# Kernel optimization log

Measured on AMD Instinct MI355X. Metric: run time of the kernel, lower is better.

Reference implementation:

```python
import jax, jax.numpy as jnp
import numpy as np

EPS = 1e-5      # eps used in abs() and log()
BN_EPS = 1e-5   # torch BatchNorm2d default eps


def setup_inputs() -> dict:
    key = jax.random.key(0)
    ks = jax.random.split(key, 5)
    N, C, F, T = 16, 4, 257, 1000
    B, K = 8, 80
    xr = jax.random.normal(ks[0], (N, C, F, T), dtype=jnp.float32)
    xi = jax.random.normal(ks[1], (N, C, F, T), dtype=jnp.float32)
    # per-bin complex beamforming weights: (F, B, C) == Conv1d weight (B*F, 1, C) regrouped
    wr = jax.random.normal(ks[2], (F, B, C), dtype=jnp.float32) * 0.25
    wi = jax.random.normal(ks[3], (F, B, C), dtype=jnp.float32) * 0.25
    # nn.Linear(num_bins, spectra_filters, bias=False) weight: (K, F)
    w_proj = jax.random.normal(ks[4], (K, F), dtype=jnp.float32) * (1.0 / np.sqrt(F))
    gamma = jnp.ones((B,), dtype=jnp.float32)
    beta = jnp.zeros((B,), dtype=jnp.float32)
    return {"xr": xr, "xi": xi, "wr": wr, "wi": wi, "w_proj": w_proj,
            "gamma": gamma, "beta": beta}


def reference(xr, xi, wr, wi, w_proj, gamma, beta):
    # Grouped complex conv1d == per-bin complex beamform across mics:
    # out[n,b,t,f] = sum_c w[f,b,c] * x[n,c,f,t] (complex product)
    br = jnp.einsum('ncft,fbc->nbtf', xr, wr) - jnp.einsum('ncft,fbc->nbtf', xi, wi)
    bi = jnp.einsum('ncft,fbc->nbtf', xi, wr) + jnp.einsum('ncft,fbc->nbtf', xr, wi)
    mag = jnp.sqrt(br * br + bi * bi + EPS)              # (N, B, T, F)
    # Linear(F -> K), ReLU, log
    f = jax.nn.relu(jnp.einsum('nbtf,kf->nbtk', mag, w_proj))
    f = jnp.log(f + EPS)                                  # (N, B, T, K)
    # BatchNorm2d over channel axis B (training-mode batch statistics)
    mean = jnp.mean(f, axis=(0, 2, 3), keepdims=True)
    var = jnp.var(f, axis=(0, 2, 3), keepdims=True)
    f = (f - mean) * jax.lax.rsqrt(var + BN_EPS)
    f = f * gamma[None, :, None, None] + beta[None, :, None, None]
    N, B, T, K = f.shape
    # (N, B, T, K) -> (N, T, B*K)
    return jnp.transpose(f, (0, 2, 1, 3)).reshape(N, T, B * K)
```

## Files before the change

### kernel.cpp

```cpp
#include <hip/hip_runtime.h>
#include <math.h>

#define N_ 16
#define C_ 4
#define F_ 257
#define T_ 1000
#define B_ 8
#define K_ 80
#define BK_ 640
#define TT_ 16
#define NT_ 63
#define NBLK (N_ * NT_)
#define MSTR 264

typedef _Float16 half4 __attribute__((ext_vector_type(4)));
typedef _Float16 half8 __attribute__((ext_vector_type(8)));
typedef float f32x4 __attribute__((ext_vector_type(4)));

#define WSCALE   256.0f
#define WUNSCALE 0.00390625f

#define WP0_OFF   0
#define WP1_OFF   (64 * 1024)
#define WP2_OFF   (128 * 1024)
#define WTAIL_OFF (192 * 1024)
#define PART_OFF  (256 * 1024)
#define SS_OFF    (PART_OFF + NBLK * 16 * 8)

__global__ __launch_bounds__(80) void k_wt(const float* __restrict__ wp,
                                           _Float16* __restrict__ wp0,
                                           _Float16* __restrict__ wp1,
                                           _Float16* __restrict__ wp2,
                                           float* __restrict__ wtail) {
    int blk = blockIdx.x;
    int tid = threadIdx.x;
    if (blk < 80) {
        if (tid < 64) {
            int ch = blk / 10, r = blk % 10, kt = r >> 1, ksub = r & 1;
            int k = kt * 16 + (tid & 15);
            int fb = ch * 32 + ksub * 16 + 4 * (tid >> 4);
#pragma unroll
            for (int j = 0; j < 4; ++j) {
                float w = wp[k * F_ + fb + j] * WSCALE;
                _Float16 w0 = (_Float16)w;
                float r1 = (w - (float)w0) * 2048.0f;
                _Float16 w1 = (_Float16)r1;
                float r2 = (r1 - (float)w1) * 2048.0f;
                _Float16 w2 = (_Float16)r2;
                size_t o = ((size_t)blk * 64 + tid) * 4 + j;
                wp0[o] = w0; wp1[o] = w1; wp2[o] = w2;
            }
        }
    } else {
        wtail[tid] = wp[tid * F_ + 256];
    }
}

__global__ __launch_bounds__(512, 2) void k_fused(
    const float* __restrict__ xr, const float* __restrict__ xi,
    const float* __restrict__ wr, const float* __restrict__ wi,
    const _Float16* __restrict__ wp0, const _Float16* __restrict__ wp1,
    const _Float16* __restrict__ wp2, const float* __restrict__ wtail,
    float* __restrict__ out, double* __restrict__ partials) {

    const int tid = threadIdx.x;
    const int bid = blockIdx.x;
    const int tt = bid % NT_;
    const int n  = bid / NT_;
    const int t0 = tt * TT_;

    __shared__ __attribute__((aligned(16))) float magS[2][TT_][MSTR];
    __shared__ __attribute__((aligned(16))) _Float16 wfS[2][3][2560];
    __shared__ float wtS[80];
    __shared__ float magT[TT_][B_];

    const int lane = tid & 63;
    const int wv   = tid >> 6;

    const int sfr = tid >> 4;
    const int t_s = tid & 15;
    const int tg  = t0 + t_s;
    const bool tld = (tg < T_);

    f32x4 accM[5], acc1[5], acc2[5];
#pragma unroll
    for (int kt = 0; kt < 5; ++kt) {
        accM[kt] = (f32x4)0.0f;
        acc1[kt] = (f32x4)0.0f;
        acc2[kt] = (f32x4)0.0f;
    }

    const float* xrn = xr + (size_t)n * C_ * F_ * T_;
    const float* xin = xi + (size_t)n * C_ * F_ * T_;

    if (tid < 80) wtS[tid] = wtail[tid];

    float pxr[C_], pxi[C_];
    if (tld) {
#pragma unroll
        for (int c = 0; c < C_; ++c) {
            pxr[c] = xrn[((size_t)c * F_ + sfr) * T_ + tg];
            pxi[c] = xin[((size_t)c * F_ + sfr) * T_ + tg];
        }
    }

    for (int ch = 0; ch < 8; ++ch) {
        const int f0 = ch * 32;
        const int f  = f0 + sfr;
        const int pb = ch & 1;

#pragma unroll
        for (int r = 0; r < 2; ++r) {
            int idx = tid + r * 512;
            if (idx < 960) {
                int term = idx / 320;
                int u = idx - term * 320;
                const _Float16* src =
                    (term == 0 ? wp0 : (term == 1 ? wp1 : wp2)) + ch * 2560 + u * 8;
                *(half8*)&wfS[pb][term][u * 8] = *(const half8*)src;
            }
        }

        {
            float m[B_];
            if (tld) {
                const float* wrp = wr + (size_t)f * B_ * C_;
                const float* wip = wi + (size_t)f * B_ * C_;
#pragma unroll
                for (int b = 0; b < B_; ++b) {
                    float4 wrv = *(const float4*)(wrp + b * C_);
                    float4 wiv = *(const float4*)(wip + b * C_);
                    float br  = pxr[0] * wrv.x + pxr[1] * wrv.y + pxr[2] * wrv.z + pxr[3] * wrv.w
                              - pxi[0] * wiv.x - pxi[1] * wiv.y - pxi[2] * wiv.z - pxi[3] * wiv.w;
                    float bi2 = pxi[0] * wrv.x + pxi[1] * wrv.y + pxi[2] * wrv.z + pxi[3] * wrv.w
                              + pxr[0] * wiv.x + pxr[1] * wiv.y + pxr[2] * wiv.z + pxr[3] * wiv.w;
                    m[b] = sqrtf(br * br + bi2 * bi2 + 1e-5f);
                }
            } else {
#pragma unroll
                for (int b = 0; b < B_; ++b) m[b] = 0.f;
            }
            *(float4*)&magS[pb][t_s][sfr * 8] = make_float4(m[0], m[1], m[2], m[3]);
            *(float4*)&magS[pb][t_s][sfr * 8 + 4] = make_float4(m[4], m[5], m[6], m[7]);
        }

        if (ch < 7 && tld) {
            const int f2 = f0 + 32 + sfr;
#pragma unroll
            for (int c = 0; c < C_; ++c) {
                pxr[c] = xrn[((size_t)c * F_ + f2) * T_ + tg];
                pxi[c] = xin[((size_t)c * F_ + f2) * T_ + tg];
            }
        }

        __syncthreads();

        {
            const int tA = lane & 15;
            const int g  = lane >> 4;
#pragma unroll
            for (int ks = 0; ks < 2; ++ks) {
                half4 a0, a1, a2;
#pragma unroll
                for (int j = 0; j < 4; ++j) {
                    float v = magS[pb][tA][(ks * 16 + 4 * g + j) * 8 + wv];
                    _Float16 h0 = (_Float16)v;
                    float r1 = (v - (float)h0) * 2048.0f;
                    _Float16 h1 = (_Float16)r1;
                    float r2 = (r1 - (float)h1) * 2048.0f;
                    a0[j] = h0; a1[j] = h1; a2[j] = (_Float16)r2;
                }
#pragma unroll
                for (int kt = 0; kt < 5; ++kt) {
                    int fi = ((kt * 2 + ks) * 64 + lane) * 4;
                    half4 b0 = *(const half4*)&wfS[pb][0][fi];
                    half4 b1 = *(const half4*)&wfS[pb][1][fi];
                    half4 b2 = *(const half4*)&wfS[pb][2][fi];
                    accM[kt] = __builtin_amdgcn_mfma_f32_16x16x16f16(a0, b0, accM[kt], 0, 0, 0);
                    acc1[kt] = __builtin_amdgcn_mfma_f32_16x16x16f16(a0, b1, acc1[kt], 0, 0, 0);
                    acc1[kt] = __builtin_amdgcn_mfma_f32_16x16x16f16(a1, b0, acc1[kt], 0, 0, 0);
                    acc2[kt] = __builtin_amdgcn_mfma_f32_16x16x16f16(a0, b2, acc2[kt], 0, 0, 0);
                    acc2[kt] = __builtin_amdgcn_mfma_f32_16x16x16f16(a1, b1, acc2[kt], 0, 0, 0);
                    acc2[kt] = __builtin_amdgcn_mfma_f32_16x16x16f16(a2, b0, acc2[kt], 0, 0, 0);
                }
            }
        }
    }

    if (tid < 128) {
        int trow = tid >> 3;
        int b = tid & 7;
        int t = t0 + trow;
        float v = 0.f;
        if (t < T_) {
            const float* wrp = wr + (size_t)(256 * B_ + b) * C_;
            const float* wip = wi + (size_t)(256 * B_ + b) * C_;
            float br = 0.f, bi2 = 0.f;
#pragma unroll
            for (int c = 0; c < C_; ++c) {
                float xrv = xrn[((size_t)c * F_ + 256) * T_ + t];
                float xiv = xin[((size_t)c * F_ + 256) * T_ + t];
                br  += xrv * wrp[c] - xiv * wip[c];
                bi2 += xiv * wrp[c] + xrv * wip[c];
            }
            v = sqrtf(br * br + bi2 * bi2 + 1e-5f);
        }
        magT[trow][b] = v;
    }
    __syncthreads();

    const int col = lane & 15;
    const int g   = lane >> 4;
    float s1 = 0.f, s2 = 0.f;
#pragma unroll
    for (int kt = 0; kt < 5; ++kt) {
        f32x4 r = (accM[kt] + 4.8828125e-4f * acc1[kt]
                   + 2.384185791015625e-7f * acc2[kt]) * WUNSCALE;
#pragma unroll
        for (int reg = 0; reg < 4; ++reg) {
            int trow = 4 * g + reg;
            int t = t0 + trow;
            float sum = r[reg] + magT[trow][wv] * wtS[kt * 16 + col];
            if (t < T_) {
                float v = fmaxf(sum, 0.0f);
                v = __logf(v + 1e-5f);
                out[((size_t)n * T_ + t) * BK_ + wv * K_ + kt * 16 + col] = v;
                s1 += v;
                s2 += v * v;
            }
        }
    }
    double d1 = (double)s1, d2 = (double)s2;
#pragma unroll
    for (int off = 32; off; off >>= 1) {
        d1 += __shfl_xor(d1, off);
        d2 += __shfl_xor(d2, off);
    }
    if (lane == 0) {
        partials[(size_t)bid * 16 + wv] = d1;
        partials[(size_t)bid * 16 + 8 + wv] = d2;
    }
}

__global__ __launch_bounds__(256) void k_bnstats(
    const double* __restrict__ partials,
    const float* __restrict__ gamma, const float* __restrict__ beta,
    float* __restrict__ ss) {
    const int b = threadIdx.x >> 5;
    const int i = threadIdx.x & 31;
    double s1 = 0.0, s2 = 0.0;
    for (int j = i; j < NBLK; j += 32) {
        s1 += partials[(size_t)j * 16 + b];
        s2 += partials[(size_t)j * 16 + 8 + b];
    }
#pragma unroll
    for (int off = 16; off; off >>= 1) {
        s1 += __shfl_down(s1, off);
        s2 += __shfl_down(s2, off);
    }
    if (i == 0) {
        const double cnt = (double)N_ * T_ * K_;
        double mean = s1 / cnt;
        double var = s2 / cnt - mean * mean;
        float scale = gamma[b] * (float)(1.0 / sqrt(var + 1e-5));
        float shift = beta[b] - (float)mean * scale;
        ss[b] = scale;
        ss[B_ + b] = shift;
    }
}

__global__ __launch_bounds__(256) void k_bnapply(float* __restrict__ out,
                                                 const float* __restrict__ ss) {
    size_t i4 = (size_t)blockIdx.x * 256 + threadIdx.x;
    int k4 = (int)(i4 % (BK_ / 4));
    int b = k4 / (K_ / 4);
    float scale = ss[b], shift = ss[B_ + b];
    float4* p = (float4*)out + i4;
    float4 v = *p;
    v.x = v.x * scale + shift;
    v.y = v.y * scale + shift;
    v.z = v.z * scale + shift;
    v.w = v.w * scale + shift;
    *p = v;
}

extern "C" void kernel_launch(void* const* d_in, const int* in_sizes, int n_in,
                              void* d_out, int out_size, void* d_ws, size_t ws_size,
                              hipStream_t stream) {
    const float* xr = (const float*)d_in[0];
    const float* xi = (const float*)d_in[1];
    const float* wr = (const float*)d_in[2];
    const float* wi = (const float*)d_in[3];
    const float* w_proj = (const float*)d_in[4];
    const float* gamma = (const float*)d_in[5];
    const float* beta = (const float*)d_in[6];
    float* out = (float*)d_out;

    _Float16* wp0 = (_Float16*)((char*)d_ws + WP0_OFF);
    _Float16* wp1 = (_Float16*)((char*)d_ws + WP1_OFF);
    _Float16* wp2 = (_Float16*)((char*)d_ws + WP2_OFF);
    float* wtail = (float*)((char*)d_ws + WTAIL_OFF);
    double* partials = (double*)((char*)d_ws + PART_OFF);
    float* ss = (float*)((char*)d_ws + SS_OFF);

    k_wt<<<81, 80, 0, stream>>>(w_proj, wp0, wp1, wp2, wtail);
    k_fused<<<NBLK, 512, 0, stream>>>(xr, xi, wr, wi, wp0, wp1, wp2, wtail, out, partials);
    k_bnstats<<<1, 256, 0, stream>>>(partials, gamma, beta, ss);
    k_bnapply<<<10000, 256, 0, stream>>>(out, ss);
}
```

Measured before the change: 171.8 us.

## Split magnitudes to fp16 triplets at producer and store in MFMA fragment layout

```diff
diff --git a/kernel.cpp b/kernel.cpp
--- a/kernel.cpp
+++ b/kernel.cpp
@@ -11,7 +11,6 @@
 #define TT_ 16
 #define NT_ 63
 #define NBLK (N_ * NT_)
-#define MSTR 264
 
 typedef _Float16 half4 __attribute__((ext_vector_type(4)));
 typedef _Float16 half8 __attribute__((ext_vector_type(8)));
@@ -69,7 +68,7 @@
     const int n  = bid / NT_;
     const int t0 = tt * TT_;
 
-    __shared__ __attribute__((aligned(16))) float magS[2][TT_][MSTR];
+    __shared__ __attribute__((aligned(16))) _Float16 aS[2][B_][2][3][256];
     __shared__ __attribute__((aligned(16))) _Float16 wfS[2][3][2560];
     __shared__ float wtS[80];
     __shared__ float magT[TT_][B_];
@@ -81,6 +80,10 @@
     const int t_s = tid & 15;
     const int tg  = t0 + t_s;
     const bool tld = (tg < T_);
+    const int a_ks = sfr >> 4;
+    const int a_g  = (sfr & 15) >> 2;
+    const int a_j  = sfr & 3;
+    const int a_off = a_g * 64 + t_s * 4 + a_j;
 
     f32x4 accM[5], acc1[5], acc2[5];
 #pragma unroll
@@ -122,26 +125,28 @@
         }
 
         {
-            float m[B_];
-            if (tld) {
-                const float* wrp = wr + (size_t)f * B_ * C_;
-                const float* wip = wi + (size_t)f * B_ * C_;
-#pragma unroll
-                for (int b = 0; b < B_; ++b) {
-                    float4 wrv = *(const float4*)(wrp + b * C_);
-                    float4 wiv = *(const float4*)(wip + b * C_);
+#pragma unroll
+            for (int b = 0; b < B_; ++b) {
+                float v = 0.f;
+                if (tld) {
+                    const float* wrp = wr + ((size_t)f * B_ + b) * C_;
+                    const float* wip = wi + ((size_t)f * B_ + b) * C_;
+                    float4 wrv = *(const float4*)wrp;
+                    float4 wiv = *(const float4*)wip;
                     float br  = pxr[0] * wrv.x + pxr[1] * wrv.y + pxr[2] * wrv.z + pxr[3] * wrv.w
                               - pxi[0] * wiv.x - pxi[1] * wiv.y - pxi[2] * wiv.z - pxi[3] * wiv.w;
                     float bi2 = pxi[0] * wrv.x + pxi[1] * wrv.y + pxi[2] * wrv.z + pxi[3] * wrv.w
                               + pxr[0] * wiv.x + pxr[1] * wiv.y + pxr[2] * wiv.z + pxr[3] * wiv.w;
-                    m[b] = sqrtf(br * br + bi2 * bi2 + 1e-5f);
+                    v = sqrtf(br * br + bi2 * bi2 + 1e-5f);
                 }
-            } else {
-#pragma unroll
-                for (int b = 0; b < B_; ++b) m[b] = 0.f;
-            }
-            *(float4*)&magS[pb][t_s][sfr * 8] = make_float4(m[0], m[1], m[2], m[3]);
-            *(float4*)&magS[pb][t_s][sfr * 8 + 4] = make_float4(m[4], m[5], m[6], m[7]);
+                _Float16 h0 = (_Float16)v;
+                float r1 = (v - (float)h0) * 2048.0f;
+                _Float16 h1 = (_Float16)r1;
+                float r2 = (r1 - (float)h1) * 2048.0f;
+                aS[pb][b][a_ks][0][a_off] = h0;
+                aS[pb][b][a_ks][1][a_off] = h1;
+                aS[pb][b][a_ks][2][a_off] = (_Float16)r2;
+            }
         }
 
         if (ch < 7 && tld) {
@@ -155,34 +160,40 @@
 
         __syncthreads();
 
-        {
-            const int tA = lane & 15;
-            const int g  = lane >> 4;
-#pragma unroll
-            for (int ks = 0; ks < 2; ++ks) {
-                half4 a0, a1, a2;
-#pragma unroll
-                for (int j = 0; j < 4; ++j) {
-                    float v = magS[pb][tA][(ks * 16 + 4 * g + j) * 8 + wv];
-                    _Float16 h0 = (_Float16)v;
-                    float r1 = (v - (float)h0) * 2048.0f;
-                    _Float16 h1 = (_Float16)r1;
-                    float r2 = (r1 - (float)h1) * 2048.0f;
-                    a0[j] = h0; a1[j] = h1; a2[j] = (_Float16)r2;
-                }
-#pragma unroll
-                for (int kt = 0; kt < 5; ++kt) {
-                    int fi = ((kt * 2 + ks) * 64 + lane) * 4;
-                    half4 b0 = *(const half4*)&wfS[pb][0][fi];
-                    half4 b1 = *(const half4*)&wfS[pb][1][fi];
-                    half4 b2 = *(const half4*)&wfS[pb][2][fi];
-                    accM[kt] = __builtin_amdgcn_mfma_f32_16x16x16f16(a0, b0, accM[kt], 0, 0, 0);
-                    acc1[kt] = __builtin_amdgcn_mfma_f32_16x16x16f16(a0, b1, acc1[kt], 0, 0, 0);
-                    acc1[kt] = __builtin_amdgcn_mfma_f32_16x16x16f16(a1, b0, acc1[kt], 0, 0, 0);
-                    acc2[kt] = __builtin_amdgcn_mfma_f32_16x16x16f16(a0, b2, acc2[kt], 0, 0, 0);
-                    acc2[kt] = __builtin_amdgcn_mfma_f32_16x16x16f16(a1, b1, acc2[kt], 0, 0, 0);
-                    acc2[kt] = __builtin_amdgcn_mfma_f32_16x16x16f16(a2, b0, acc2[kt], 0, 0, 0);
-                }
+#pragma unroll
+        for (int ks = 0; ks < 2; ++ks) {
+            half4 a0 = *(const half4*)&aS[pb][wv][ks][0][lane * 4];
+            half4 a1 = *(const half4*)&aS[pb][wv][ks][1][lane * 4];
+            half4 a2 = *(const half4*)&aS[pb][wv][ks][2][lane * 4];
+#pragma unroll
+            for (int kt = 0; kt < 5; ++kt) {
+                half4 b0 = *(const half4*)&wfS[pb][0][((kt * 2 + ks) * 64 + lane) * 4];
+                accM[kt] = __builtin_amdgcn_mfma_f32_16x16x16f16(a0, b0, accM[kt], 0, 0, 0);
+            }
+#pragma unroll
+            for (int kt = 0; kt < 5; ++kt) {
+                half4 b1 = *(const half4*)&wfS[pb][1][((kt * 2 + ks) * 64 + lane) * 4];
+                acc1[kt] = __builtin_amdgcn_mfma_f32_16x16x16f16(a0, b1, acc1[kt], 0, 0, 0);
+            }
+#pragma unroll
+            for (int kt = 0; kt < 5; ++kt) {
+                half4 b0 = *(const half4*)&wfS[pb][0][((kt * 2 + ks) * 64 + lane) * 4];
+                acc1[kt] = __builtin_amdgcn_mfma_f32_16x16x16f16(a1, b0, acc1[kt], 0, 0, 0);
+            }
+#pragma unroll
+            for (int kt = 0; kt < 5; ++kt) {
+                half4 b2 = *(const half4*)&wfS[pb][2][((kt * 2 + ks) * 64 + lane) * 4];
+                acc2[kt] = __builtin_amdgcn_mfma_f32_16x16x16f16(a0, b2, acc2[kt], 0, 0, 0);
+            }
+#pragma unroll
+            for (int kt = 0; kt < 5; ++kt) {
+                half4 b1 = *(const half4*)&wfS[pb][1][((kt * 2 + ks) * 64 + lane) * 4];
+                acc2[kt] = __builtin_amdgcn_mfma_f32_16x16x16f16(a1, b1, acc2[kt], 0, 0, 0);
+            }
+#pragma unroll
+            for (int kt = 0; kt < 5; ++kt) {
+                half4 b0 = *(const half4*)&wfS[pb][0][((kt * 2 + ks) * 64 + lane) * 4];
+                acc2[kt] = __builtin_amdgcn_mfma_f32_16x16x16f16(a2, b0, acc2[kt], 0, 0, 0);
             }
         }
     }
```

After: 185.4 us. +7.9%, slower.

## Split fused beamform+projection kernel into magnitude kernel and per-wave GEMM kernel

Applied to the files above, without the earlier changes.

```diff
diff --git a/kernel.cpp b/kernel.cpp
--- a/kernel.cpp
+++ b/kernel.cpp
@@ -11,10 +11,9 @@
 #define TT_ 16
 #define NT_ 63
 #define NBLK (N_ * NT_)
-#define MSTR 264
+#define NWAVE (NBLK * B_)
 
 typedef _Float16 half4 __attribute__((ext_vector_type(4)));
-typedef _Float16 half8 __attribute__((ext_vector_type(8)));
 typedef float f32x4 __attribute__((ext_vector_type(4)));
 
 #define WSCALE   256.0f
@@ -24,8 +23,10 @@
 #define WP1_OFF   (64 * 1024)
 #define WP2_OFF   (128 * 1024)
 #define WTAIL_OFF (192 * 1024)
-#define PART_OFF  (256 * 1024)
-#define SS_OFF    (PART_OFF + NBLK * 16 * 8)
+#define MAGT_OFF  (256 * 1024)
+#define PART_OFF  (1024 * 1024)
+#define SS_OFF    (PART_OFF + NWAVE * 2 * 8)
+#define MAGF_OFF  (2 * 1024 * 1024)
 
 __global__ __launch_bounds__(80) void k_wt(const float* __restrict__ wp,
                                            _Float16* __restrict__ wp0,
@@ -56,12 +57,10 @@
     }
 }
 
-__global__ __launch_bounds__(512, 2) void k_fused(
+__global__ __launch_bounds__(512) void k_mag(
     const float* __restrict__ xr, const float* __restrict__ xi,
     const float* __restrict__ wr, const float* __restrict__ wi,
-    const _Float16* __restrict__ wp0, const _Float16* __restrict__ wp1,
-    const _Float16* __restrict__ wp2, const float* __restrict__ wtail,
-    float* __restrict__ out, double* __restrict__ partials) {
+    float* __restrict__ magF, float* __restrict__ magT) {
 
     const int tid = threadIdx.x;
     const int bid = blockIdx.x;
@@ -69,31 +68,15 @@
     const int n  = bid / NT_;
     const int t0 = tt * TT_;
 
-    __shared__ __attribute__((aligned(16))) float magS[2][TT_][MSTR];
-    __shared__ __attribute__((aligned(16))) _Float16 wfS[2][3][2560];
-    __shared__ float wtS[80];
-    __shared__ float magT[TT_][B_];
-
-    const int lane = tid & 63;
-    const int wv   = tid >> 6;
-
     const int sfr = tid >> 4;
     const int t_s = tid & 15;
     const int tg  = t0 + t_s;
     const bool tld = (tg < T_);
-
-    f32x4 accM[5], acc1[5], acc2[5];
-#pragma unroll
-    for (int kt = 0; kt < 5; ++kt) {
-        accM[kt] = (f32x4)0.0f;
-        acc1[kt] = (f32x4)0.0f;
-        acc2[kt] = (f32x4)0.0f;
-    }
+    const int a_ks = sfr >> 4;
+    const int a_off = ((sfr & 15) >> 2) * 64 + t_s * 4 + (sfr & 3);
 
     const float* xrn = xr + (size_t)n * C_ * F_ * T_;
     const float* xin = xi + (size_t)n * C_ * F_ * T_;
-
-    if (tid < 80) wtS[tid] = wtail[tid];
 
     float pxr[C_], pxi[C_];
     if (tld) {
@@ -105,86 +88,37 @@
     }
 
     for (int ch = 0; ch < 8; ++ch) {
-        const int f0 = ch * 32;
-        const int f  = f0 + sfr;
-        const int pb = ch & 1;
-
-#pragma unroll
-        for (int r = 0; r < 2; ++r) {
-            int idx = tid + r * 512;
-            if (idx < 960) {
-                int term = idx / 320;
-                int u = idx - term * 320;
-                const _Float16* src =
-                    (term == 0 ? wp0 : (term == 1 ? wp1 : wp2)) + ch * 2560 + u * 8;
-                *(half8*)&wfS[pb][term][u * 8] = *(const half8*)src;
-            }
-        }
-
-        {
-            float m[B_];
-            if (tld) {
-                const float* wrp = wr + (size_t)f * B_ * C_;
-                const float* wip = wi + (size_t)f * B_ * C_;
-#pragma unroll
-                for (int b = 0; b < B_; ++b) {
-                    float4 wrv = *(const float4*)(wrp + b * C_);
-                    float4 wiv = *(const float4*)(wip + b * C_);
-                    float br  = pxr[0] * wrv.x + pxr[1] * wrv.y + pxr[2] * wrv.z + pxr[3] * wrv.w
-                              - pxi[0] * wiv.x - pxi[1] * wiv.y - pxi[2] * wiv.z - pxi[3] * wiv.w;
-                    float bi2 = pxi[0] * wrv.x + pxi[1] * wrv.y + pxi[2] * wrv.z + pxi[3] * wrv.w
-                              + pxr[0] * wiv.x + pxr[1] * wiv.y + pxr[2] * wiv.z + pxr[3] * wiv.w;
-                    m[b] = sqrtf(br * br + bi2 * bi2 + 1e-5f);
-                }
-            } else {
-#pragma unroll
-                for (int b = 0; b < B_; ++b) m[b] = 0.f;
-            }
-            *(float4*)&magS[pb][t_s][sfr * 8] = make_float4(m[0], m[1], m[2], m[3]);
-            *(float4*)&magS[pb][t_s][sfr * 8 + 4] = make_float4(m[4], m[5], m[6], m[7]);
-        }
-
+        const int f = ch * 32 + sfr;
+        float m[B_];
+        if (tld) {
+            const float* wrp = wr + (size_t)f * B_ * C_;
+            const float* wip = wi + (size_t)f * B_ * C_;
+#pragma unroll
+            for (int b = 0; b < B_; ++b) {
+                float4 wrv = *(const float4*)(wrp + b * C_);
+                float4 wiv = *(const float4*)(wip + b * C_);
+                float br  = pxr[0] * wrv.x + pxr[1] * wrv.y + pxr[2] * wrv.z + pxr[3] * wrv.w
+                          - pxi[0] * wiv.x - pxi[1] * wiv.y - pxi[2] * wiv.z - pxi[3] * wiv.w;
+                float bi2 = pxi[0] * wrv.x + pxi[1] * wrv.y + pxi[2] * wrv.z + pxi[3] * wrv.w
+                          + pxr[0] * wiv.x + pxr[1] * wiv.y + pxr[2] * wiv.z + pxr[3] * wiv.w;
+                m[b] = sqrtf(br * br + bi2 * bi2 + 1e-5f);
+            }
+        } else {
+#pragma unroll
+            for (int b = 0; b < B_; ++b) m[b] = 0.f;
+        }
         if (ch < 7 && tld) {
-            const int f2 = f0 + 32 + sfr;
+            const int f2 = (ch + 1) * 32 + sfr;
 #pragma unroll
             for (int c = 0; c < C_; ++c) {
                 pxr[c] = xrn[((size_t)c * F_ + f2) * T_ + tg];
                 pxi[c] = xin[((size_t)c * F_ + f2) * T_ + tg];
             }
         }
-
-        __syncthreads();
-
-        {
-            const int tA = lane & 15;
-            const int g  = lane >> 4;
-#pragma unroll
-            for (int ks = 0; ks < 2; ++ks) {
-                half4 a0, a1, a2;
-#pragma unroll
-                for (int j = 0; j < 4; ++j) {
-                    float v = magS[pb][tA][(ks * 16 + 4 * g + j) * 8 + wv];
-                    _Float16 h0 = (_Float16)v;
-                    float r1 = (v - (float)h0) * 2048.0f;
-                    _Float16 h1 = (_Float16)r1;
-                    float r2 = (r1 - (float)h1) * 2048.0f;
-                    a0[j] = h0; a1[j] = h1; a2[j] = (_Float16)r2;
-                }
-#pragma unroll
-                for (int kt = 0; kt < 5; ++kt) {
-                    int fi = ((kt * 2 + ks) * 64 + lane) * 4;
-                    half4 b0 = *(const half4*)&wfS[pb][0][fi];
-                    half4 b1 = *(const half4*)&wfS[pb][1][fi];
-                    half4 b2 = *(const half4*)&wfS[pb][2][fi];
-                    accM[kt] = __builtin_amdgcn_mfma_f32_16x16x16f16(a0, b0, accM[kt], 0, 0, 0);
-                    acc1[kt] = __builtin_amdgcn_mfma_f32_16x16x16f16(a0, b1, acc1[kt], 0, 0, 0);
-                    acc1[kt] = __builtin_amdgcn_mfma_f32_16x16x16f16(a1, b0, acc1[kt], 0, 0, 0);
-                    acc2[kt] = __builtin_amdgcn_mfma_f32_16x16x16f16(a0, b2, acc2[kt], 0, 0, 0);
-                    acc2[kt] = __builtin_amdgcn_mfma_f32_16x16x16f16(a1, b1, acc2[kt], 0, 0, 0);
-                    acc2[kt] = __builtin_amdgcn_mfma_f32_16x16x16f16(a2, b0, acc2[kt], 0, 0, 0);
-                }
-            }
-        }
+        size_t base = ((((size_t)bid * B_) * 8 + ch) * 2 + a_ks) * 256 + a_off;
+#pragma unroll
+        for (int b = 0; b < B_; ++b)
+            magF[base + (size_t)b * 4096] = m[b];
     }
 
     if (tid < 128) {
@@ -205,9 +139,80 @@
             }
             v = sqrtf(br * br + bi2 * bi2 + 1e-5f);
         }
-        magT[trow][b] = v;
-    }
-    __syncthreads();
+        magT[(size_t)bid * TT_ * B_ + trow * B_ + b] = v;
+    }
+}
+
+__global__ __launch_bounds__(64) void k_gemm(
+    const float* __restrict__ magF,
+    const _Float16* __restrict__ wp0, const _Float16* __restrict__ wp1,
+    const _Float16* __restrict__ wp2, const float* __restrict__ wtail,
+    const float* __restrict__ magT,
+    float* __restrict__ out, double* __restrict__ partials) {
+
+    const int wid = blockIdx.x;
+    const int b   = wid & 7;
+    const int nt  = wid >> 3;
+    const int tt  = nt % NT_;
+    const int n   = nt / NT_;
+    const int t0  = tt * TT_;
+    const int lane = threadIdx.x;
+
+    f32x4 accM[5], acc1[5], acc2[5];
+#pragma unroll
+    for (int kt = 0; kt < 5; ++kt) {
+        accM[kt] = (f32x4)0.0f;
+        acc1[kt] = (f32x4)0.0f;
+        acc2[kt] = (f32x4)0.0f;
+    }
+
+    for (int ch = 0; ch < 8; ++ch) {
+#pragma unroll
+        for (int ks = 0; ks < 2; ++ks) {
+            f32x4 mv = *(const f32x4*)&magF[((((size_t)wid) * 8 + ch) * 2 + ks) * 256 + lane * 4];
+            half4 a0, a1, a2;
+#pragma unroll
+            for (int j = 0; j < 4; ++j) {
+                float v = mv[j];
+                _Float16 h0 = (_Float16)v;
+                float r1 = (v - (float)h0) * 2048.0f;
+                _Float16 h1 = (_Float16)r1;
+                float r2 = (r1 - (float)h1) * 2048.0f;
+                a0[j] = h0; a1[j] = h1; a2[j] = (_Float16)r2;
+            }
+            const int fb = (ch * 10 + ks) * 64 + lane;
+#pragma unroll
+            for (int kt = 0; kt < 5; ++kt) {
+                half4 b0 = *(const half4*)&wp0[(size_t)(fb + kt * 128) * 4];
+                accM[kt] = __builtin_amdgcn_mfma_f32_16x16x16f16(a0, b0, accM[kt], 0, 0, 0);
+            }
+#pragma unroll
+            for (int kt = 0; kt < 5; ++kt) {
+                half4 b1 = *(const half4*)&wp1[(size_t)(fb + kt * 128) * 4];
+                acc1[kt] = __builtin_amdgcn_mfma_f32_16x16x16f16(a0, b1, acc1[kt], 0, 0, 0);
+            }
+#pragma unroll
+            for (int kt = 0; kt < 5; ++kt) {
+                half4 b0 = *(const half4*)&wp0[(size_t)(fb + kt * 128) * 4];
+                acc1[kt] = __builtin_amdgcn_mfma_f32_16x16x16f16(a1, b0, acc1[kt], 0, 0, 0);
+            }
+#pragma unroll
+            for (int kt = 0; kt < 5; ++kt) {
+                half4 b2 = *(const half4*)&wp2[(size_t)(fb + kt * 128) * 4];
+                acc2[kt] = __builtin_amdgcn_mfma_f32_16x16x16f16(a0, b2, acc2[kt], 0, 0, 0);
+            }
+#pragma unroll
+            for (int kt = 0; kt < 5; ++kt) {
+                half4 b1 = *(const half4*)&wp1[(size_t)(fb + kt * 128) * 4];
+                acc2[kt] = __builtin_amdgcn_mfma_f32_16x16x16f16(a1, b1, acc2[kt], 0, 0, 0);
+            }
+#pragma unroll
+            for (int kt = 0; kt < 5; ++kt) {
+                half4 b0 = *(const half4*)&wp0[(size_t)(fb + kt * 128) * 4];
+                acc2[kt] = __builtin_amdgcn_mfma_f32_16x16x16f16(a2, b0, acc2[kt], 0, 0, 0);
+            }
+        }
+    }
 
     const int col = lane & 15;
     const int g   = lane >> 4;
@@ -220,11 +225,12 @@
         for (int reg = 0; reg < 4; ++reg) {
             int trow = 4 * g + reg;
             int t = t0 + trow;
-            float sum = r[reg] + magT[trow][wv] * wtS[kt * 16 + col];
+            float sum = r[reg] + magT[(size_t)nt * TT_ * B_ + trow * B_ + b]
+                                  * wtail[kt * 16 + col];
             if (t < T_) {
                 float v = fmaxf(sum, 0.0f);
                 v = __logf(v + 1e-5f);
-                out[((size_t)n * T_ + t) * BK_ + wv * K_ + kt * 16 + col] = v;
+                out[((size_t)n * T_ + t) * BK_ + b * K_ + kt * 16 + col] = v;
                 s1 += v;
                 s2 += v * v;
             }
@@ -237,8 +243,8 @@
         d2 += __shfl_xor(d2, off);
     }
     if (lane == 0) {
-        partials[(size_t)bid * 16 + wv] = d1;
-        partials[(size_t)bid * 16 + 8 + wv] = d2;
+        partials[(size_t)wid * 2]     = d1;
+        partials[(size_t)wid * 2 + 1] = d2;
     }
 }
 
@@ -250,8 +256,8 @@
     const int i = threadIdx.x & 31;
     double s1 = 0.0, s2 = 0.0;
     for (int j = i; j < NBLK; j += 32) {
-        s1 += partials[(size_t)j * 16 + b];
-        s2 += partials[(size_t)j * 16 + 8 + b];
+        s1 += partials[((size_t)j * 8 + b) * 2];
+        s2 += partials[((size_t)j * 8 + b) * 2 + 1];
     }
 #pragma unroll
     for (int off = 16; off; off >>= 1) {
@@ -300,11 +306,14 @@
     _Float16* wp1 = (_Float16*)((char*)d_ws + WP1_OFF);
     _Float16* wp2 = (_Float16*)((char*)d_ws + WP2_OFF);
     float* wtail = (float*)((char*)d_ws + WTAIL_OFF);
+    float* magT = (float*)((char*)d_ws + MAGT_OFF);
     double* partials = (double*)((char*)d_ws + PART_OFF);
     float* ss = (float*)((char*)d_ws + SS_OFF);
+    float* magF = (float*)((char*)d_ws + MAGF_OFF);
 
     k_wt<<<81, 80, 0, stream>>>(w_proj, wp0, wp1, wp2, wtail);
-    k_fused<<<NBLK, 512, 0, stream>>>(xr, xi, wr, wi, wp0, wp1, wp2, wtail, out, partials);
+    k_mag<<<NBLK, 512, 0, stream>>>(xr, xi, wr, wi, magF, magT);
+    k_gemm<<<NWAVE, 64, 0, stream>>>(magF, wp0, wp1, wp2, wtail, magT, out, partials);
     k_bnstats<<<1, 256, 0, stream>>>(partials, gamma, beta, ss);
     k_bnapply<<<10000, 256, 0, stream>>>(out, ss);
 }
```

Measured after the change: 206.1 us. 1.2x slower.
